# Kernel tuning notes

Measured on AMD Instinct MI355X. Metric: run time of the kernel, lower is better.

The kernel has to match this reference:

```python
import jax, jax.numpy as jnp
import numpy as np

B, T, N_EMBD = 1, 2048, 2048
N_HEAD = 16
KV_LOW = 512      # kv_low_rank == head_size (compressed value dim)
Q_LOW = 1024
ROPE_HS = 64
QK_HS = KV_LOW + ROPE_HS  # 576
HEAD_SIZE = KV_LOW        # v_equiv = c_kv.view(B,1,T,head_size)


def _rope_tables(seq_len, dim, base=10000.0):
    # litgpt-style: theta over half dim, duplicated to full dim
    inv = 1.0 / (base ** (np.arange(0, dim, 2, dtype=np.float32) / dim))
    t = np.arange(seq_len, dtype=np.float32)
    freqs = np.outer(t, inv)                      # [T, dim/2]
    emb = np.concatenate([freqs, freqs], axis=-1)  # [T, dim]
    return jnp.asarray(np.cos(emb)), jnp.asarray(np.sin(emb))


def _apply_rope(x, cos, sin):
    # x: [..., T, d]; cos/sin broadcastable [T, d]. rotate-half RoPE.
    d = x.shape[-1]
    x1, x2 = x[..., : d // 2], x[..., d // 2:]
    rotated = jnp.concatenate([-x2, x1], axis=-1)
    return x * cos + rotated * sin


def setup_inputs() -> dict:
    key = jax.random.key(0)
    ks = jax.random.split(key, 4)
    x = jax.random.normal(ks[0], (B, T, N_EMBD), dtype=jnp.float32)
    cos, sin = _rope_tables(T, ROPE_HS)
    s = 0.02
    W_qkv = jax.random.normal(ks[1], (N_EMBD, KV_LOW + ROPE_HS + Q_LOW), dtype=jnp.float32) * s
    W_qdec = jax.random.normal(ks[2], (Q_LOW, N_HEAD * QK_HS), dtype=jnp.float32) * s
    W_out = jax.random.normal(ks[3], (N_HEAD * HEAD_SIZE, N_EMBD), dtype=jnp.float32) * s
    return {"x": x, "cos": cos, "sin": sin, "W_qkv": W_qkv, "W_qdec": W_qdec, "W_out": W_out}


def reference(x, cos, sin, W_qkv, W_qdec, W_out):
    Bq, Tq, _ = x.shape
    # latent encoding and split
    latents = x @ W_qkv                                       # [B,T,kv+rope+q]
    c_kv = latents[..., :KV_LOW]                              # [B,T,512] (keys-nope and values)
    k_r = latents[..., KV_LOW:KV_LOW + ROPE_HS]               # [B,T,64]
    c_q = latents[..., KV_LOW + ROPE_HS:]                     # [B,T,1024]
    # per-head query decode
    q = (c_q @ W_qdec).reshape(Bq, Tq, N_HEAD, QK_HS)         # [B,T,H,576]
    q_nope, q_r = q[..., :KV_LOW], q[..., KV_LOW:]
    # partial RoPE
    k_r = _apply_rope(k_r, cos, sin)                          # [B,T,64]
    q_r = _apply_rope(q_r, cos[None, :, None, :], sin[None, :, None, :])  # [B,T,H,64]
    q = jnp.concatenate([q_nope, q_r], axis=-1)               # [B,T,H,576]
    q = jnp.swapaxes(q, 1, 2)                                 # [B,H,T,576]
    k = jnp.concatenate([c_kv, k_r], axis=-1)                 # [B,T,576] shared across heads
    v = c_kv                                                  # [B,T,512] shared across heads
    scale = 1.0 / jnp.sqrt(jnp.float32(HEAD_SIZE))
    scores = jnp.einsum('bhtd,bsd->bhts', q, k) * scale       # [B,H,T,T]
    causal = jnp.tril(jnp.ones((Tq, Tq), dtype=bool))
    scores = jnp.where(causal, scores, jnp.finfo(scores.dtype).min)
    attn = jax.nn.softmax(scores, axis=-1)
    y = jnp.einsum('bhts,bsd->bhtd', attn, v)                 # [B,H,T,512]
    y = jnp.swapaxes(y, 1, 2).reshape(Bq, Tq, N_HEAD * HEAD_SIZE)
    return y @ W_out                                          # [B,T,n_embd]
```

## Files before the change

### kernel.cpp

```cpp
#include <hip/hip_runtime.h>

typedef __bf16 bf16x8_t __attribute__((ext_vector_type(8)));
typedef float f32x4_t __attribute__((ext_vector_type(4)));

#define LAT_LD 1664
#define QK_DIM 576
#define V_DIM 512
#define NHEAD 16
#define TSEQ 2048
#define QLD 9216
#define YLD 8192
#define KLD 576
#define SCALE 0.044194173824159216f

__device__ __forceinline__ unsigned short f2bf(float f) {
  union { float f; unsigned int u; } v; v.f = f;
  unsigned int r = v.u + 0x7FFFu + ((v.u >> 16) & 1u);
  return (unsigned short)(r >> 16);
}

__device__ __forceinline__ void load_lds16(const unsigned short* g, unsigned short* l) {
  __builtin_amdgcn_global_load_lds((const __attribute__((address_space(1))) void*)g,
                                   (__attribute__((address_space(3))) void*)l, 16, 0, 0);
}

__device__ __forceinline__ void conv_t_body(const float* __restrict__ src, int R, int Csrc,
                                            unsigned short* __restrict__ dst,
                                            int bx, int by, int tid,
                                            unsigned short (*T)[72]) {
  const int r0 = bx * 64, c0 = by * 64;
  const bool live = (c0 < Csrc);
#pragma unroll
  for (int it = 0; it < 4; ++it) {
    int idx = it * 256 + tid;
    int r = idx >> 4, c4 = (idx & 15) * 4;
    float4 v = {0.f, 0.f, 0.f, 0.f};
    if (live) v = *(const float4*)&src[(size_t)(r0 + r) * Csrc + c0 + c4];
    T[c4 + 0][r] = f2bf(v.x);
    T[c4 + 1][r] = f2bf(v.y);
    T[c4 + 2][r] = f2bf(v.z);
    T[c4 + 3][r] = f2bf(v.w);
  }
  __syncthreads();
#pragma unroll
  for (int it = 0; it < 2; ++it) {
    int idx = it * 256 + tid;
    int cc = idx >> 3, r8 = (idx & 7) * 8;
    uint4 v = *(const uint4*)&T[cc][r8];
    *(uint4*)&dst[(size_t)(c0 + cc) * R + r0 + r8] = v;
  }
}

__global__ __launch_bounds__(256) void prep_all(
    const float* __restrict__ x, unsigned short* __restrict__ xb,
    const float* __restrict__ wqkv, unsigned short* __restrict__ wqkvT,
    const float* __restrict__ wqdec, unsigned short* __restrict__ wqdecT,
    const float* __restrict__ wout, unsigned short* __restrict__ woutT,
    float* __restrict__ lsum) {
  __shared__ unsigned short T[64][72];
  const int blk = blockIdx.x, tid = threadIdx.x;
  if (blk < 4096) {
    int i = (blk * 256 + tid) * 4;
    float4 v = *(const float4*)&x[i];
    ushort4 o;
    o.x = f2bf(v.x); o.y = f2bf(v.y); o.z = f2bf(v.z); o.w = f2bf(v.w);
    *(ushort4*)&xb[i] = o;
  } else if (blk < 4928) {
    int l = blk - 4096;
    conv_t_body(wqkv, 2048, 1600, wqkvT, l & 31, l >> 5, tid, T);
  } else if (blk < 7232) {
    int l = blk - 4928;
    conv_t_body(wqdec, 1024, 9216, wqdecT, l & 15, l >> 4, tid, T);
  } else if (blk < 11328) {
    int l = blk - 7232;
    conv_t_body(wout, 8192, 2048, woutT, l & 127, l >> 7, tid, T);
  } else {
    int i = ((blk - 11328) * 256 + tid) * 4;
    *(float4*)&lsum[i] = (float4){0.f, 0.f, 0.f, 0.f};
  }
}

__global__ __launch_bounds__(256) void postlat(
    const float* __restrict__ P1,
    unsigned short* __restrict__ lat,
    unsigned short* __restrict__ kbuf,
    unsigned short* __restrict__ vtg,
    const float* __restrict__ cosb, const float* __restrict__ sinb) {
  __shared__ unsigned short T[64][72];
  const int tid = threadIdx.x;
  const int bx = blockIdx.x, by = blockIdx.y;
  const int r0 = bx * 64, c0 = by * 64;
  const size_t n = (size_t)2048 * 1664;

#pragma unroll
  for (int it = 0; it < 4; ++it) {
    int idx = it * 256 + tid;
    int r = idx >> 4, c4 = (idx & 15) * 4;
    size_t off = (size_t)(r0 + r) * 1664 + c0 + c4;
    float4 a = *(const float4*)&P1[off];
    float4 b = *(const float4*)&P1[n + off];
    ushort4 o;
    o.x = f2bf(a.x + b.x); o.y = f2bf(a.y + b.y);
    o.z = f2bf(a.z + b.z); o.w = f2bf(a.w + b.w);
    if (by < 8) {
      *(ushort4*)&kbuf[(size_t)(r0 + r) * KLD + c0 + c4] = o;
      T[c4 + 0][r] = o.x; T[c4 + 1][r] = o.y; T[c4 + 2][r] = o.z; T[c4 + 3][r] = o.w;
    } else if (by == 8) {
      T[r][c4 + 0] = o.x; T[r][c4 + 1] = o.y; T[r][c4 + 2] = o.z; T[r][c4 + 3] = o.w;
    } else {
      *(ushort4*)&lat[(size_t)(r0 + r) * LAT_LD + c0 + c4] = o;
    }
  }
  if (by > 8) return;
  __syncthreads();
  if (by < 8) {
#pragma unroll
    for (int it = 0; it < 2; ++it) {
      int idx = it * 256 + tid;
      int cc = idx >> 3, r8 = (idx & 7) * 8;
      uint4 v = *(const uint4*)&T[cc][r8];
      *(uint4*)&vtg[(size_t)(c0 + cc) * TSEQ + r0 + r8] = v;
    }
  } else {
#pragma unroll
    for (int it = 0; it < 8; ++it) {
      int idx = it * 256 + tid;
      int r = idx >> 5, d = idx & 31;
      int t = r0 + r;
      union { unsigned int u; float f; } a, b;
      a.u = ((unsigned int)T[r][d]) << 16;
      b.u = ((unsigned int)T[r][d + 32]) << 16;
      float c0f = cosb[t * 64 + d], s0f = sinb[t * 64 + d];
      float c1f = cosb[t * 64 + d + 32], s1f = sinb[t * 64 + d + 32];
      kbuf[(size_t)t * KLD + 512 + d] = f2bf(a.f * c0f - b.f * s0f);
      kbuf[(size_t)t * KLD + 544 + d] = f2bf(b.f * c1f + a.f * s1f);
    }
  }
}

#define GEMM_PROLOGUE()                                                     \
  __shared__ __align__(16) unsigned short As[8192];                         \
  __shared__ __align__(16) unsigned short Bs[8192];                         \
  const int tid = threadIdx.x;                                              \
  const int wave = tid >> 6, lane = tid & 63;                               \
  const int quad = lane >> 4, l16 = lane & 15;                              \
  const int wm = wave >> 1, wn = wave & 1;                                  \
  f32x4_t acc[4][4];                                                        \
  f32x4_t zero = {0.f, 0.f, 0.f, 0.f};                                      \
  _Pragma("unroll") for (int mi = 0; mi < 4; ++mi)                          \
    _Pragma("unroll") for (int ni = 0; ni < 4; ++ni) acc[mi][ni] = zero;

#define GEMM_KLOOP(Aptr, Alda, Bptr, Bldb, M0, N0, KLEN)                    \
  for (int k0 = 0; k0 < (KLEN); k0 += 64) {                                 \
    _Pragma("unroll") for (int p2 = 0; p2 < 2; ++p2) {                      \
      int ci = p2 * 256 + tid;                                              \
      int rr2 = ci >> 2, cc2 = (ci & 3) * 8;                                \
      const unsigned short* ga = &(Aptr)[(size_t)((M0) + rr2) * (Alda) + k0 + cc2]; \
      const unsigned short* gb = &(Bptr)[(size_t)((N0) + rr2) * (Bldb) + k0 + cc2]; \
      load_lds16(ga,      &As[ci * 8]);                                     \
      load_lds16(ga + 32, &As[4096 + ci * 8]);                              \
      load_lds16(gb,      &Bs[ci * 8]);                                     \
      load_lds16(gb + 32, &Bs[4096 + ci * 8]);                              \
    }                                                                       \
    __syncthreads();                                                        \
    _Pragma("unroll") for (int hf = 0; hf < 2; ++hf) {                      \
      bf16x8_t af[4], bfr[4];                                               \
      _Pragma("unroll") for (int mi = 0; mi < 4; ++mi)                      \
        af[mi] = *(const bf16x8_t*)&As[hf * 4096 + (wm * 64 + mi * 16 + l16) * 32 + quad * 8]; \
      _Pragma("unroll") for (int ni = 0; ni < 4; ++ni)                      \
        bfr[ni] = *(const bf16x8_t*)&Bs[hf * 4096 + (wn * 64 + ni * 16 + l16) * 32 + quad * 8]; \
      _Pragma("unroll") for (int mi = 0; mi < 4; ++mi)                      \
        _Pragma("unroll") for (int ni = 0; ni < 4; ++ni)                    \
          acc[mi][ni] = __builtin_amdgcn_mfma_f32_16x16x32_bf16(af[mi], bfr[ni], acc[mi][ni], 0, 0, 0); \
    }                                                                       \
    __syncthreads();                                                        \
  }

__global__ __launch_bounds__(256, 2) void gemm_splitk(
    const unsigned short* __restrict__ A, int lda,
    const unsigned short* __restrict__ Bt, int ldb,
    float* __restrict__ P, int ldc, int Ks) {
  const int m0 = blockIdx.y * 128, n0 = blockIdx.x * 128;
  const size_t koff = (size_t)blockIdx.z * Ks;
  const unsigned short* Ap = A + koff;
  const unsigned short* Bp = Bt + koff;
  float* C = P + (size_t)blockIdx.z * ((size_t)gridDim.y * 128) * ldc;
  GEMM_PROLOGUE();
  GEMM_KLOOP(Ap, lda, Bp, ldb, m0, n0, Ks);
#pragma unroll
  for (int mi = 0; mi < 4; ++mi)
#pragma unroll
    for (int ni = 0; ni < 4; ++ni)
#pragma unroll
      for (int r = 0; r < 4; ++r) {
        int row = m0 + wm * 64 + mi * 16 + quad * 4 + r;
        int col = n0 + wn * 64 + ni * 16 + l16;
        C[(size_t)row * ldc + col] = acc[mi][ni][r];
      }
}

__global__ __launch_bounds__(256, 2) void gemm_qdec(
    const unsigned short* __restrict__ A,
    const unsigned short* __restrict__ Bt,
    unsigned short* __restrict__ qbuf,
    const float* __restrict__ cosb, const float* __restrict__ sinb) {
  const int m0 = blockIdx.y * 128, n0 = blockIdx.x * 128;
  GEMM_PROLOGUE();
  GEMM_KLOOP(A, LAT_LD, Bt, 1024, m0, n0, 1024);

  const int cb = n0 + wn * 64;
  const bool ropeh = (cb % QK_DIM) == 512;
#pragma unroll
  for (int mi = 0; mi < 4; ++mi)
#pragma unroll
    for (int r = 0; r < 4; ++r) {
      int t = m0 + wm * 64 + mi * 16 + quad * 4 + r;
      if (ropeh) {
#pragma unroll
        for (int ni = 0; ni < 2; ++ni) {
          int d = ni * 16 + l16;
          float c0f = cosb[t * 64 + d], s0f = sinb[t * 64 + d];
          float c1f = cosb[t * 64 + d + 32], s1f = sinb[t * 64 + d + 32];
          float v1 = acc[mi][ni][r], v2 = acc[mi][ni + 2][r];
          qbuf[(size_t)t * QLD + cb + d] = f2bf(v1 * c0f - v2 * s0f);
          qbuf[(size_t)t * QLD + cb + 32 + d] = f2bf(v2 * c1f + v1 * s1f);
        }
      } else {
#pragma unroll
        for (int ni = 0; ni < 4; ++ni)
          qbuf[(size_t)t * QLD + cb + ni * 16 + l16] = f2bf(acc[mi][ni][r]);
      }
    }
}

#define SWZ(o) ((o) ^ ((((o) >> 7) & 7) << 4))
#define SBAR() do { __builtin_amdgcn_s_barrier(); __builtin_amdgcn_sched_barrier(0); } while (0)
#define VMCNT(n) asm volatile("s_waitcnt vmcnt(" #n ")" ::: "memory")

__device__ __forceinline__ bf16x8_t frag_ld256(const unsigned short* region, int rl, int kk, int quad) {
  int lin = rl * 128 + kk * 64 + quad * 16;
  lin ^= (rl & 7) << 4;
  return *(const bf16x8_t*)((const unsigned char*)region + lin);
}

__device__ __forceinline__ void stg256(
    const unsigned short* __restrict__ A, int lda, int m0,
    const unsigned short* __restrict__ Bt, int ldb, int n0,
    unsigned short* lds, int k, int r, int NT,
    int srow0, int scol0, int srow1, int scol1, int tid) {
  if (k >= NT) return;
  unsigned short* dst = lds + ((k & 1) << 15) + (r << 13);
  const unsigned short* g = (r < 2) ? A : Bt;
  const int ld = (r < 2) ? lda : ldb;
  const int rb = ((r < 2) ? m0 : n0) + (r & 1) * 128;
  const int c0 = k * 64;
  load_lds16(g + (size_t)(rb + srow0) * ld + c0 + scol0, dst + tid * 8);
  load_lds16(g + (size_t)(rb + srow1) * ld + c0 + scol1, dst + 4096 + tid * 8);
}

#define MFMAQ(MB, NB, BREG)                                                 \
  __builtin_amdgcn_s_setprio(1);                                            \
  _Pragma("unroll") for (int mi = 0; mi < 4; ++mi)                          \
    _Pragma("unroll") for (int ni = 0; ni < 2; ++ni)                        \
      _Pragma("unroll") for (int kk = 0; kk < 2; ++kk)                      \
        acc[(MB) + mi][(NB) + ni] = __builtin_amdgcn_mfma_f32_16x16x32_bf16( \
            a[mi][kk], BREG[ni][kk], acc[(MB) + mi][(NB) + ni], 0, 0, 0);    \
  __builtin_amdgcn_s_setprio(0);

#define STG(k, r) stg256(A, lda, m0, Bt, ldb, n0, lds, (k), (r), NT, srow0, scol0, srow1, scol1, tid)

__device__ __forceinline__ void kloop256(
    const unsigned short* __restrict__ A, int lda, int m0,
    const unsigned short* __restrict__ Bt, int ldb, int n0,
    int NT, unsigned short* lds, f32x4_t (&acc)[8][4],
    int tid, int quad, int l16, int wm, int wn) {
  const int o0 = tid * 16, o1 = 8192 + tid * 16;
  const int so0 = SWZ(o0), so1 = SWZ(o1);
  const int srow0 = so0 >> 7, scol0 = (so0 & 127) >> 1;
  const int srow1 = so1 >> 7, scol1 = (so1 & 127) >> 1;
  STG(0, 0); STG(0, 1); STG(0, 2); STG(0, 3);
  STG(1, 0); STG(1, 1); STG(1, 2); STG(1, 3);
  if (NT >= 2) { VMCNT(8); } else { VMCNT(0); }
  SBAR();
  const int brow = (wn & 1) * 64;
  for (int t = 0; t < NT; ++t) {
    const unsigned short* Ar = lds + ((t & 1) << 15) + (wm << 13);
    const unsigned short* Br = lds + ((t & 1) << 15) + 16384 + ((wn >> 1) << 13);
    bf16x8_t a[4][2], b0[2][2], b1[2][2];
#pragma unroll
    for (int mi = 0; mi < 4; ++mi) {
      a[mi][0] = frag_ld256(Ar, mi * 16 + l16, 0, quad);
      a[mi][1] = frag_ld256(Ar, mi * 16 + l16, 1, quad);
    }
#pragma unroll
    for (int ni = 0; ni < 2; ++ni) {
      b0[ni][0] = frag_ld256(Br, brow + ni * 16 + l16, 0, quad);
      b0[ni][1] = frag_ld256(Br, brow + ni * 16 + l16, 1, quad);
    }
    MFMAQ(0, 0, b0);
#pragma unroll
    for (int ni = 0; ni < 2; ++ni) {
      b1[ni][0] = frag_ld256(Br, brow + (2 + ni) * 16 + l16, 0, quad);
      b1[ni][1] = frag_ld256(Br, brow + (2 + ni) * 16 + l16, 1, quad);
    }
    MFMAQ(0, 2, b1);
    SBAR();
#pragma unroll
    for (int mi = 0; mi < 4; ++mi) {
      a[mi][0] = frag_ld256(Ar, (4 + mi) * 16 + l16, 0, quad);
      a[mi][1] = frag_ld256(Ar, (4 + mi) * 16 + l16, 1, quad);
    }
    STG(t + 2, 2); STG(t + 2, 3);
    MFMAQ(4, 2, b1);
    SBAR();
    STG(t + 2, 0); STG(t + 2, 1);
    MFMAQ(4, 0, b0);
    if (t < NT - 2) { VMCNT(8); }
    else if (t == NT - 2) { VMCNT(0); }
    SBAR();
  }
}

__global__ __launch_bounds__(512, 2) void gemm256_splitk(
    const unsigned short* __restrict__ A, int lda,
    const unsigned short* __restrict__ Bt, int ldb,
    float* __restrict__ P, int ldc, int Ks) {
  __shared__ __align__(16) unsigned short lds[65536];
  const int tid = threadIdx.x;
  const int quad = (tid >> 4) & 3, l16 = tid & 15;
  const int wave = tid >> 6, wm = wave >> 2, wn = wave & 3;
  const int m0 = blockIdx.y * 256, n0 = blockIdx.x * 256;
  const unsigned short* Ap = A + (size_t)blockIdx.z * Ks;
  const unsigned short* Bp = Bt + (size_t)blockIdx.z * Ks;
  float* C = P + (size_t)blockIdx.z * ((size_t)gridDim.y * 256) * ldc;
  f32x4_t acc[8][4];
  f32x4_t z4 = {0.f, 0.f, 0.f, 0.f};
#pragma unroll
  for (int mi = 0; mi < 8; ++mi)
#pragma unroll
    for (int ni = 0; ni < 4; ++ni) acc[mi][ni] = z4;
  kloop256(Ap, lda, m0, Bp, ldb, n0, Ks >> 6, lds, acc, tid, quad, l16, wm, wn);
#pragma unroll
  for (int mi = 0; mi < 8; ++mi)
#pragma unroll
    for (int ni = 0; ni < 4; ++ni)
#pragma unroll
      for (int r = 0; r < 4; ++r) {
        const int row = m0 + wm * 128 + mi * 16 + quad * 4 + r;
        const int col = n0 + wn * 64 + ni * 16 + l16;
        C[(size_t)row * ldc + col] = acc[mi][ni][r];
      }
}

__global__ __launch_bounds__(256) void reduce4_f32(const float* __restrict__ p,
                                                   float* __restrict__ dst, int n) {
  int i = (blockIdx.x * 256 + threadIdx.x) * 4;
  if (i < n) {
    float4 a = *(const float4*)&p[i];
    float4 b = *(const float4*)&p[(size_t)n + i];
    float4 c = *(const float4*)&p[2 * (size_t)n + i];
    float4 d = *(const float4*)&p[3 * (size_t)n + i];
    float4 o;
    o.x = (a.x + b.x) + (c.x + d.x);
    o.y = (a.y + b.y) + (c.y + d.y);
    o.z = (a.z + b.z) + (c.z + d.z);
    o.w = (a.w + b.w) + (c.w + d.w);
    *(float4*)&dst[i] = o;
  }
}

__global__ __launch_bounds__(256, 2) void qke_kernel(
    const unsigned short* __restrict__ qbuf,
    const unsigned short* __restrict__ kbuf,
    unsigned short* __restrict__ Ebuf,
    float* __restrict__ lsum, int hbase) {
  const int id = blockIdx.x + 136 * blockIdx.y;
  const int wg = (id & 7) * 136 + (id >> 3);
  int tx = wg % 136;
  const int hl = wg / 136;
  int ig = 15, cnt = 16;
  while (tx >= cnt) { tx -= cnt; --ig; --cnt; }
  const int j = tx;
  const int h = hbase + hl;
  const int Kmax = (ig + 1) << 7;
  const int r0g = ig << 7;
  const int pre = (ig * (ig + 1)) >> 1;

  const unsigned short* A = qbuf + (size_t)r0g * QLD + h * QK_DIM;
  const unsigned short* Bt = kbuf + (size_t)(j << 7) * KLD;
  unsigned short* Eh = Ebuf + ((size_t)hl * 136 + pre) * 16384;

  GEMM_PROLOGUE();
  GEMM_KLOOP(A, QLD, Bt, KLD, 0, 0, QK_DIM);

#pragma unroll
  for (int mi = 0; mi < 4; ++mi) {
    float rs[4] = {0.f, 0.f, 0.f, 0.f};
#pragma unroll
    for (int ni = 0; ni < 4; ++ni)
#pragma unroll
      for (int r = 0; r < 4; ++r) {
        int qr = r0g + wm * 64 + mi * 16 + quad * 4 + r;
        int key = (j << 7) + wn * 64 + ni * 16 + l16;
        float e = (key <= qr) ? __expf(acc[mi][ni][r] * SCALE) : 0.f;
        rs[r] += e;
        Eh[(size_t)(qr - r0g) * Kmax + key] = f2bf(e);
      }
#pragma unroll
    for (int r = 0; r < 4; ++r) {
      float s = rs[r];
#pragma unroll
      for (int off = 1; off < 16; off <<= 1) s += __shfl_xor(s, off, 64);
      if (l16 == 0) {
        int qr = r0g + wm * 64 + mi * 16 + quad * 4 + r;
        atomicAdd(&lsum[h * TSEQ + qr], s);
      }
    }
  }
}

__global__ __launch_bounds__(256, 2) void pv_kernel(
    const unsigned short* __restrict__ Ebuf,
    const unsigned short* __restrict__ vtg,
    const float* __restrict__ lsum,
    unsigned short* __restrict__ ybuf, int hbase) {
  const int id = blockIdx.x + 4 * blockIdx.y + 64 * blockIdx.z;
  const int wg = (id & 7) * 64 + (id >> 3);
  const int ig = 15 - ((wg >> 2) & 15);
  const int hl = wg >> 6, h = hbase + hl;
  const int n0 = (wg & 3) * 128;
  const int Kmax = (ig + 1) << 7;
  const int pre = (ig * (ig + 1)) >> 1;

  const unsigned short* A = Ebuf + ((size_t)hl * 136 + pre) * 16384;

  GEMM_PROLOGUE();
  GEMM_KLOOP(A, Kmax, vtg, TSEQ, 0, n0, Kmax);

#pragma unroll
  for (int mi = 0; mi < 4; ++mi)
#pragma unroll
    for (int r = 0; r < 4; ++r) {
      int row_g = (ig << 7) + wm * 64 + mi * 16 + quad * 4 + r;
      float inv = 1.f / lsum[h * TSEQ + row_g];
#pragma unroll
      for (int ni = 0; ni < 4; ++ni) {
        int col = h * V_DIM + n0 + wn * 64 + ni * 16 + l16;
        ybuf[(size_t)row_g * YLD + col] = f2bf(acc[mi][ni][r] * inv);
      }
    }
}

extern "C" void kernel_launch(void* const* d_in, const int* in_sizes, int n_in,
                              void* d_out, int out_size, void* d_ws, size_t ws_size,
                              hipStream_t stream) {
  (void)in_sizes; (void)n_in; (void)out_size; (void)ws_size;
  const float* x     = (const float*)d_in[0];
  const float* cosb  = (const float*)d_in[1];
  const float* sinb  = (const float*)d_in[2];
  const float* wqkv  = (const float*)d_in[3];
  const float* wqdec = (const float*)d_in[4];
  const float* wout  = (const float*)d_in[5];
  float* out = (float*)d_out;

  unsigned short* ws     = (unsigned short*)d_ws;
  unsigned short* xb     = ws;
  unsigned short* wqkvT  = xb     + (size_t)2048 * 2048;
  unsigned short* wqdecT = wqkvT  + (size_t)1664 * 2048;
  unsigned short* lat    = wqdecT + (size_t)9216 * 1024;
  unsigned short* qbuf   = lat    + (size_t)2048 * 1664;
  unsigned short* woutT  = qbuf   + (size_t)2048 * 9216;
  unsigned short* ybuf   = woutT  + (size_t)2048 * 8192;
  unsigned short* vtg    = ybuf   + (size_t)2048 * 8192;
  unsigned short* kbuf   = vtg    + (size_t)512 * 2048;
  float*          lsumf  = (float*)(kbuf + (size_t)2048 * 576);
  unsigned short* Ebuf   = ws;
  float*          P1     = (float*)qbuf;
  float*          Pf     = (float*)ws;

  prep_all<<<11360, 256, 0, stream>>>(x, xb, wqkv, wqkvT, wqdec, wqdecT, wout, woutT, lsumf);

  gemm_splitk<<<dim3(13, 16, 2), 256, 0, stream>>>(xb, 2048, wqkvT, 2048, P1, 1664, 1024);
  postlat<<<dim3(32, 26), 256, 0, stream>>>(P1, lat, kbuf, vtg, cosb, sinb);

  gemm_qdec<<<dim3(72, 16), 256, 0, stream>>>(lat + 576, wqdecT, qbuf, cosb, sinb);

  qke_kernel<<<dim3(136, 8), 256, 0, stream>>>(qbuf, kbuf, Ebuf, lsumf, 0);
  pv_kernel<<<dim3(4, 16, 8), 256, 0, stream>>>(Ebuf, vtg, lsumf, ybuf, 0);
  qke_kernel<<<dim3(136, 8), 256, 0, stream>>>(qbuf, kbuf, Ebuf, lsumf, 8);
  pv_kernel<<<dim3(4, 16, 8), 256, 0, stream>>>(Ebuf, vtg, lsumf, ybuf, 8);

  gemm256_splitk<<<dim3(8, 8, 4), 512, 0, stream>>>(ybuf, 8192, woutT, 8192, Pf, 2048, 2048);
  reduce4_f32<<<4096, 256, 0, stream>>>(Pf, out, 2048 * 2048);
}
```

Before: 480.1 us.

## Use 256x256 tiles for causal QK^T exp kernel with matching E layout

```diff
diff --git a/kernel.cpp b/kernel.cpp
--- a/kernel.cpp
+++ b/kernel.cpp
@@ -369,42 +369,51 @@
   }
 }
 
-__global__ __launch_bounds__(256, 2) void qke_kernel(
+__global__ __launch_bounds__(512, 2) void qke256_kernel(
     const unsigned short* __restrict__ qbuf,
     const unsigned short* __restrict__ kbuf,
     unsigned short* __restrict__ Ebuf,
     float* __restrict__ lsum, int hbase) {
-  const int id = blockIdx.x + 136 * blockIdx.y;
-  const int wg = (id & 7) * 136 + (id >> 3);
-  int tx = wg % 136;
-  const int hl = wg / 136;
-  int ig = 15, cnt = 16;
+  __shared__ __align__(16) unsigned short lds[65536];
+  const int tid = threadIdx.x;
+  const int quad = (tid >> 4) & 3, l16 = tid & 15;
+  const int wave = tid >> 6, wm = wave >> 2, wn = wave & 3;
+  const int id = blockIdx.x + 36 * blockIdx.y;
+  const int wg = (id & 7) * 36 + (id >> 3);
+  int tx = wg % 36;
+  const int hl = wg / 36;
+  int ig = 7, cnt = 8;
   while (tx >= cnt) { tx -= cnt; --ig; --cnt; }
   const int j = tx;
   const int h = hbase + hl;
-  const int Kmax = (ig + 1) << 7;
-  const int r0g = ig << 7;
+  const int Kmax = (ig + 1) << 8;
   const int pre = (ig * (ig + 1)) >> 1;
 
-  const unsigned short* A = qbuf + (size_t)r0g * QLD + h * QK_DIM;
-  const unsigned short* Bt = kbuf + (size_t)(j << 7) * KLD;
-  unsigned short* Eh = Ebuf + ((size_t)hl * 136 + pre) * 16384;
-
-  GEMM_PROLOGUE();
-  GEMM_KLOOP(A, QLD, Bt, KLD, 0, 0, QK_DIM);
-
-#pragma unroll
-  for (int mi = 0; mi < 4; ++mi) {
+  const unsigned short* A = qbuf + (size_t)(ig << 8) * QLD + h * QK_DIM;
+  const unsigned short* Bt = kbuf + (size_t)(j << 8) * KLD;
+  unsigned short* Eh = Ebuf + ((size_t)hl * 36 + pre) * 65536;
+
+  f32x4_t acc[8][4];
+  f32x4_t z4 = {0.f, 0.f, 0.f, 0.f};
+#pragma unroll
+  for (int mi = 0; mi < 8; ++mi)
+#pragma unroll
+    for (int ni = 0; ni < 4; ++ni) acc[mi][ni] = z4;
+  kloop256(A, QLD, 0, Bt, KLD, 0, QK_DIM >> 6, lds, acc, tid, quad, l16, wm, wn);
+
+#pragma unroll
+  for (int mi = 0; mi < 8; ++mi) {
     float rs[4] = {0.f, 0.f, 0.f, 0.f};
 #pragma unroll
     for (int ni = 0; ni < 4; ++ni)
 #pragma unroll
       for (int r = 0; r < 4; ++r) {
-        int qr = r0g + wm * 64 + mi * 16 + quad * 4 + r;
-        int key = (j << 7) + wn * 64 + ni * 16 + l16;
-        float e = (key <= qr) ? __expf(acc[mi][ni][r] * SCALE) : 0.f;
+        const int rloc = wm * 128 + mi * 16 + quad * 4 + r;
+        const int row_g = (ig << 8) + rloc;
+        const int key = (j << 8) + wn * 64 + ni * 16 + l16;
+        float e = (key <= row_g) ? __expf(acc[mi][ni][r] * SCALE) : 0.f;
         rs[r] += e;
-        Eh[(size_t)(qr - r0g) * Kmax + key] = f2bf(e);
+        Eh[(size_t)rloc * Kmax + key] = f2bf(e);
       }
 #pragma unroll
     for (int r = 0; r < 4; ++r) {
@@ -412,8 +421,8 @@
 #pragma unroll
       for (int off = 1; off < 16; off <<= 1) s += __shfl_xor(s, off, 64);
       if (l16 == 0) {
-        int qr = r0g + wm * 64 + mi * 16 + quad * 4 + r;
-        atomicAdd(&lsum[h * TSEQ + qr], s);
+        const int row_g = (ig << 8) + wm * 128 + mi * 16 + quad * 4 + r;
+        atomicAdd(&lsum[h * TSEQ + row_g], s);
       }
     }
   }
@@ -426,13 +435,15 @@
     unsigned short* __restrict__ ybuf, int hbase) {
   const int id = blockIdx.x + 4 * blockIdx.y + 64 * blockIdx.z;
   const int wg = (id & 7) * 64 + (id >> 3);
-  const int ig = 15 - ((wg >> 2) & 15);
+  const int qt = 15 - ((wg >> 2) & 15);
   const int hl = wg >> 6, h = hbase + hl;
   const int n0 = (wg & 3) * 128;
-  const int Kmax = (ig + 1) << 7;
+  const int ig = qt >> 1, sub = qt & 1;
+  const int Kmax = (ig + 1) << 8;
   const int pre = (ig * (ig + 1)) >> 1;
 
-  const unsigned short* A = Ebuf + ((size_t)hl * 136 + pre) * 16384;
+  const unsigned short* A = Ebuf + ((size_t)hl * 36 + pre) * 65536
+                          + (size_t)sub * 128 * Kmax;
 
   GEMM_PROLOGUE();
   GEMM_KLOOP(A, Kmax, vtg, TSEQ, 0, n0, Kmax);
@@ -441,7 +452,7 @@
   for (int mi = 0; mi < 4; ++mi)
 #pragma unroll
     for (int r = 0; r < 4; ++r) {
-      int row_g = (ig << 7) + wm * 64 + mi * 16 + quad * 4 + r;
+      int row_g = (qt << 7) + wm * 64 + mi * 16 + quad * 4 + r;
       float inv = 1.f / lsum[h * TSEQ + row_g];
 #pragma unroll
       for (int ni = 0; ni < 4; ++ni) {
@@ -485,9 +496,9 @@
 
   gemm_qdec<<<dim3(72, 16), 256, 0, stream>>>(lat + 576, wqdecT, qbuf, cosb, sinb);
 
-  qke_kernel<<<dim3(136, 8), 256, 0, stream>>>(qbuf, kbuf, Ebuf, lsumf, 0);
+  qke256_kernel<<<dim3(36, 8), 512, 0, stream>>>(qbuf, kbuf, Ebuf, lsumf, 0);
   pv_kernel<<<dim3(4, 16, 8), 256, 0, stream>>>(Ebuf, vtg, lsumf, ybuf, 0);
-  qke_kernel<<<dim3(136, 8), 256, 0, stream>>>(qbuf, kbuf, Ebuf, lsumf, 8);
+  qke256_kernel<<<dim3(36, 8), 512, 0, stream>>>(qbuf, kbuf, Ebuf, lsumf, 8);
   pv_kernel<<<dim3(4, 16, 8), 256, 0, stream>>>(Ebuf, vtg, lsumf, ybuf, 8);
 
   gemm256_splitk<<<dim3(8, 8, 4), 512, 0, stream>>>(ybuf, 8192, woutT, 8192, Pf, 2048, 2048);
```

Result: slower. 540.4 us (+12.6%).
